# Kernel optimization log

Measured on AMD Instinct MI355X. Metric: run time of the kernel, lower is better.

The kernel has to match this reference:

```python
import jax, jax.numpy as jnp
import numpy as np

HIDDEN = 1024
NEG_INF = jnp.float32(-1e7)


def setup_inputs() -> dict:
    key = jax.random.key(0)
    ks = jax.random.split(key, 9)
    B, S, H = 4, 2048, HIDDEN
    std = 1.0 / np.sqrt(H)
    return {
        "queries": jax.random.normal(ks[0], (B, S, H), jnp.float32),
        "keys": jax.random.normal(ks[1], (B, S, H), jnp.float32),
        "values": jax.random.normal(ks[2], (B, S, H), jnp.float32),
        "Wq": jax.random.uniform(ks[3], (H, H), jnp.float32, -std, std),
        "bq": jax.random.uniform(ks[4], (H,), jnp.float32, -std, std),
        "Wk": jax.random.uniform(ks[5], (H, H), jnp.float32, -std, std),
        "bk": jax.random.uniform(ks[6], (H,), jnp.float32, -std, std),
        "Wv": jax.random.uniform(ks[7], (H, H), jnp.float32, -std, std),
        "bv": jax.random.uniform(ks[8], (H,), jnp.float32, -std, std),
    }


def reference(queries, keys, values, Wq, bq, Wk, bk, Wv, bv):
    # q,k,v: (B, S, H) linear projections (torch Linear: x @ W.T + b)
    q = jnp.einsum('bth,oh->bto', queries, Wq) + bq
    k = jnp.einsum('bsh,oh->bso', keys, Wk) + bk
    v = jnp.einsum('bsh,oh->bso', values, Wv) + bv
    scale = jax.lax.rsqrt(jnp.float32(q.shape[-1] * 0 + Wq.shape[0]))
    # scores[b, s, t] = <k_s, q_t> * scale   (key index s, query index t)
    scores = jnp.einsum('bsh,bth->bst', k, q) * scale
    S, T = scores.shape[1], scores.shape[2]
    # torch.tril(ones * -1e7, diagonal=-1): add -1e7 where s > t (strictly lower)
    mask = jnp.where(jnp.arange(S)[:, None] > jnp.arange(T)[None, :], NEG_INF, 0.0)
    attn = jax.nn.softmax(scores + mask, axis=1)  # softmax over key dim (dim=1)
    context = jnp.einsum('bst,bsh->bth', attn, v)  # (B, T, H)
    return context, attn
```

## Files before the change

kernel.cpp:

```cpp
#include <hip/hip_runtime.h>
#include <math.h>

typedef __bf16 bf16x8 __attribute__((ext_vector_type(8)));
typedef __bf16 bf16x4 __attribute__((ext_vector_type(4)));
typedef float f32x4 __attribute__((ext_vector_type(4)));

#define HD 1024
#define SEQ 2048
#define NB 4
#define WEL (HD * HD)

__device__ inline bf16x8 load8cvt(const __bf16* p) { return *(const bf16x8*)p; }
__device__ inline bf16x8 load8cvt(const float* p) {
    f32x4 a = *(const f32x4*)p;
    f32x4 b = *(const f32x4*)(p + 4);
    bf16x8 r;
#pragma unroll
    for (int i = 0; i < 4; ++i) { r[i] = (__bf16)a[i]; r[i + 4] = (__bf16)b[i]; }
    return r;
}

__device__ inline f32x4 load4f(const float* p) { return *(const f32x4*)p; }
__device__ inline f32x4 load4f(const __bf16* p) {
    bf16x4 v = *(const bf16x4*)p;
    f32x4 r;
#pragma unroll
    for (int i = 0; i < 4; ++i) r[i] = (float)v[i];
    return r;
}

__device__ inline void gld_lds16(const void* g, void* l) {
    __builtin_amdgcn_global_load_lds(
        (const __attribute__((address_space(1))) unsigned int*)g,
        (__attribute__((address_space(3))) unsigned int*)l, 16, 0, 0);
}

template <typename T>
__device__ inline void stage_tile(const T* __restrict__ G, int ld, __bf16* s, int tid)
{
    const int r  = tid >> 3;
    const int co = ((tid & 7) ^ (r & 7)) * 8;
    if constexpr (sizeof(T) == 2) {
        __bf16* dst = s + (tid >> 6) * 512;
#pragma unroll
        for (int c = 0; c < 4; ++c)
            gld_lds16(G + (long)(c * 32 + r) * ld + co, dst + c * 2048);
    } else {
#pragma unroll
        for (int c = 0; c < 4; ++c)
            *(bf16x8*)(s + c * 2048 + tid * 8) = load8cvt(G + (long)(c * 32 + r) * ld + co);
    }
}

__device__ inline bf16x8 frag_read(const __bf16* s, int row, int c)
{
    return *(const bf16x8*)&s[row * 64 + ((c ^ (row & 7)) * 8)];
}

__device__ inline void mfma_ktile(const __bf16* __restrict__ sa,
                                  const __bf16* __restrict__ sb,
                                  int wm, int wn, int l15, int quad,
                                  f32x4 (&acc)[4][4])
{
#pragma unroll
    for (int kk = 0; kk < 64; kk += 32) {
        const int c8 = quad + (kk >> 3);
        bf16x8 af[4], bf[4];
#pragma unroll
        for (int i = 0; i < 4; ++i)
            af[i] = frag_read(sa, wm + i * 16 + l15, c8);
#pragma unroll
        for (int j = 0; j < 4; ++j)
            bf[j] = frag_read(sb, wn + j * 16 + l15, c8);
#pragma unroll
        for (int i = 0; i < 4; ++i)
#pragma unroll
            for (int j = 0; j < 4; ++j)
                acc[i][j] = __builtin_amdgcn_mfma_f32_16x16x32_bf16(af[i], bf[j], acc[i][j], 0, 0, 0);
    }
}

struct Proj3 {
    const void* A[3];
    const void* W[3];
    const float* bias[3];
    __bf16* C[3];
    int vtmask;
};

template <typename TA, typename TW>
__global__ __launch_bounds__(256) void gemm_proj(Proj3 p)
{
    __shared__ __bf16 sA[2][128 * 64];
    __shared__ __bf16 sB[2][128 * 64];

    const int tid = threadIdx.x;
    const int L = blockIdx.x;
    const int per = gridDim.x >> 3;
    const int wrk = (L & 7) * per + (L >> 3);
    const int n0 = (wrk & 7) * 128;
    const int m0 = ((wrk >> 3) & 63) * 128;
    const int z  = wrk >> 9;
    const bool vt = (p.vtmask >> z) & 1;

    const TA* Ag = (const TA*)p.A[z] + (long)m0 * HD;
    const TW* Wg = (const TW*)p.W[z] + (long)n0 * HD;
    const float* bias = p.bias[z];
    __bf16* C = p.C[z];

    const int lane = tid & 63;
    const int l15  = lane & 15;
    const int quad = lane >> 4;
    const int wave = tid >> 6;
    const int wm = (wave >> 1) * 64;
    const int wn = (wave & 1) * 64;

    f32x4 acc[4][4];
    const f32x4 zero = {0.f, 0.f, 0.f, 0.f};
#pragma unroll
    for (int i = 0; i < 4; ++i)
#pragma unroll
        for (int j = 0; j < 4; ++j) acc[i][j] = zero;

    stage_tile(Ag, HD, sA[0], tid);
    stage_tile(Wg, HD, sB[0], tid);
    __syncthreads();

    int cur = 0;
    for (int kc = 0; kc < HD; kc += 64) {
        const int nxt = kc + 64;
        if (nxt < HD) {
            stage_tile(Ag + nxt, HD, sA[cur ^ 1], tid);
            stage_tile(Wg + nxt, HD, sB[cur ^ 1], tid);
        }
        mfma_ktile(sA[cur], sB[cur], wm, wn, l15, quad, acc);
        __syncthreads();
        cur ^= 1;
    }

#pragma unroll
    for (int j = 0; j < 4; ++j) {
        const int col = n0 + wn + j * 16 + l15;
        const float bv = bias[col];
#pragma unroll
        for (int i = 0; i < 4; ++i) {
#pragma unroll
            for (int r = 0; r < 4; ++r) {
                const int row = m0 + wm + i * 16 + quad * 4 + r;
                const float v = acc[i][j][r] + bv;
                if (vt) {
                    C[(((long)(row >> 11) * HD) + col) * SEQ + (row & (SEQ - 1))] = (__bf16)v;
                } else {
                    C[(long)row * HD + col] = (__bf16)v;
                }
            }
        }
    }
}

template <bool TRI, bool CKLIM, bool EXPSUM, typename OutT>
__global__ __launch_bounds__(256) void gemm_bt(
    const __bf16* __restrict__ A, long strideA, int lda,
    const __bf16* __restrict__ B, long strideB, int ldb,
    OutT* __restrict__ C, long strideC, int ldc,
    float* __restrict__ gsum,
    int K, float alpha)
{
    __shared__ __bf16 sA[2][128 * 64];
    __shared__ __bf16 sB[2][128 * 64];
    __shared__ float csum[128];

    const int tid = threadIdx.x;
    const int L = blockIdx.x;
    const int per = gridDim.x >> 3;
    const int wrk = (L & 7) * per + (L >> 3);
    int n0, m0, z;
    if (TRI) {
        const int Lt = wrk % 136;
        z = wrk / 136;
        int tb = (int)((sqrtf(8.f * Lt + 1.f) - 1.f) * 0.5f);
        while ((tb + 1) * (tb + 2) / 2 <= Lt) ++tb;
        while (tb * (tb + 1) / 2 > Lt) --tb;
        const int sb = Lt - tb * (tb + 1) / 2;
        n0 = tb * 128;
        m0 = sb * 128;
    } else {
        n0 = (wrk & 7) * 128;
        m0 = ((wrk >> 3) & 15) * 128;
        z  = wrk >> 7;
    }

    const __bf16* Ag = A + (long)z * strideA + (long)m0 * lda;
    const __bf16* Bg = B + (long)z * strideB + (long)n0 * ldb;
    C += (long)z * strideC;
    if (EXPSUM) {
        gsum += (long)z * SEQ;
        if (tid < 128) csum[tid] = 0.f;
    }

    const int lane = tid & 63;
    const int l15  = lane & 15;
    const int quad = lane >> 4;
    const int wave = tid >> 6;
    const int wm = (wave >> 1) * 64;
    const int wn = (wave & 1) * 64;

    f32x4 acc[4][4];
    const f32x4 zero = {0.f, 0.f, 0.f, 0.f};
#pragma unroll
    for (int i = 0; i < 4; ++i)
#pragma unroll
        for (int j = 0; j < 4; ++j) acc[i][j] = zero;

    const int Kend = CKLIM ? min(K, m0 + 128) : K;

    stage_tile(Ag, lda, sA[0], tid);
    stage_tile(Bg, ldb, sB[0], tid);
    __syncthreads();

    int cur = 0;
    for (int kc = 0; kc < Kend; kc += 64) {
        const int nxt = kc + 64;
        if (nxt < Kend) {
            stage_tile(Ag + nxt, lda, sA[cur ^ 1], tid);
            stage_tile(Bg + nxt, ldb, sB[cur ^ 1], tid);
        }
        mfma_ktile(sA[cur], sB[cur], wm, wn, l15, quad, acc);
        __syncthreads();
        cur ^= 1;
    }

#pragma unroll
    for (int j = 0; j < 4; ++j) {
        const int col = n0 + wn + j * 16 + l15;
        float part = 0.f;
#pragma unroll
        for (int i = 0; i < 4; ++i) {
#pragma unroll
            for (int r = 0; r < 4; ++r) {
                const int row = m0 + wm + i * 16 + quad * 4 + r;
                float v = acc[i][j][r] * alpha;
                if (EXPSUM) {
                    v = __expf(v);
                    if (row <= col) part += v;
                }
                C[(long)row * ldc + col] = (OutT)v;
            }
        }
        if (EXPSUM) atomicAdd(&csum[wn + j * 16 + l15], part);
    }
    if (EXPSUM) {
        __syncthreads();
        if (tid < 128) atomicAdd(&gsum[n0 + tid], csum[tid]);
    }
}

template <typename ET>
__global__ __launch_bounds__(256) void scale_emit(
    const ET* __restrict__ E, float* __restrict__ Out,
    const float* __restrict__ csum, __bf16* __restrict__ AT)
{
    __shared__ __bf16 tile[64][65];
    const int b = blockIdx.z;
    const int t0 = blockIdx.x * 128;
    const int s0 = blockIdx.y * 128;
    const ET* Eb = E + (long)b * SEQ * SEQ;
    float* Ob = Out + (long)b * SEQ * SEQ;
    __bf16* Ab = AT + (long)b * SEQ * SEQ;
    const int tid = threadIdx.x;

    if (s0 > t0 + 127) {
        const f32x4 z4 = {0.f, 0.f, 0.f, 0.f};
        const int c4 = (tid & 31) * 4;
        for (int r = tid >> 5; r < 128; r += 8)
            *(f32x4*)&Ob[(long)(s0 + r) * SEQ + t0 + c4] = z4;
        return;
    }

#pragma unroll
    for (int ds = 0; ds < 2; ++ds) {
#pragma unroll
        for (int dt = 0; dt < 2; ++dt) {
            const int ss = s0 + ds * 64, tt = t0 + dt * 64;
            const int c4 = (tid & 15) * 4;
            const int tcol = tt + c4;
            const f32x4 sv = *(const f32x4*)&csum[(long)b * SEQ + tcol];
            f32x4 inv;
#pragma unroll
            for (int k = 0; k < 4; ++k) inv[k] = 1.0f / sv[k];
#pragma unroll
            for (int r0 = 0; r0 < 64; r0 += 16) {
                const int s = ss + r0 + (tid >> 4);
                f32x4 e = load4f(&Eb[(long)s * SEQ + tcol]);
                f32x4 p;
#pragma unroll
                for (int k = 0; k < 4; ++k)
                    p[k] = (s <= tcol + k) ? e[k] * inv[k] : 0.f;
                *(f32x4*)&Ob[(long)s * SEQ + tcol] = p;
#pragma unroll
                for (int k = 0; k < 4; ++k)
                    tile[r0 + (tid >> 4)][c4 + k] = (__bf16)p[k];
            }
            __syncthreads();
            const int tr = tid >> 2;
            const int sc = (tid & 3) * 16;
            __bf16 v[16];
#pragma unroll
            for (int jj = 0; jj < 16; ++jj) v[jj] = tile[sc + jj][tr];
            *(bf16x8*)&Ab[(long)(tt + tr) * SEQ + ss + sc]     = *(bf16x8*)v;
            *(bf16x8*)&Ab[(long)(tt + tr) * SEQ + ss + sc + 8] = *(bf16x8*)(v + 8);
            __syncthreads();
        }
    }
}

struct CvtJob { const float* in; __bf16* out; int nblk; };
struct Cvt6 { CvtJob j[6]; };
__global__ __launch_bounds__(256) void cvt_bf16(Cvt6 c)
{
    const CvtJob jb = c.j[blockIdx.y];
    if ((int)blockIdx.x >= jb.nblk) return;
    const long i = ((long)blockIdx.x * 256 + threadIdx.x) * 8;
    *(bf16x8*)&jb.out[i] = load8cvt(&jb.in[i]);
}

extern "C" void kernel_launch(void* const* d_in, const int* in_sizes, int n_in,
                              void* d_out, int out_size, void* d_ws, size_t ws_size,
                              hipStream_t stream)
{
    const float* queries = (const float*)d_in[0];
    const float* keys    = (const float*)d_in[1];
    const float* values  = (const float*)d_in[2];
    const float* Wq = (const float*)d_in[3];
    const float* bq = (const float*)d_in[4];
    const float* Wk = (const float*)d_in[5];
    const float* bk = (const float*)d_in[6];
    const float* Wv = (const float*)d_in[7];
    const float* bv = (const float*)d_in[8];

    const long tokens = (long)NB * SEQ;
    const long pe = tokens * HD;
    const size_t SLOT = (size_t)pe * sizeof(__bf16);
    const int ABLK = (int)(pe / 2048);
    const int WBLK = WEL / 2048;

    float* outCtx  = (float*)d_out;
    float* outAttn = outCtx + tokens * HD;
    float* colsum = outCtx;
    __bf16* wb = (__bf16*)outAttn;
    __bf16* Wqb = wb, *Wkb = wb + WEL, *Wvb = wb + 2 * WEL;

    const dim3 blk(256);
    hipMemsetAsync(colsum, 0, (size_t)NB * SEQ * sizeof(float), stream);

    char* w = (char*)d_ws;
    __bf16 *qp, *kp, *vT, *attnT;

    bool ebig = false;
    __bf16* Ebf = nullptr;

    if (ws_size >= 6 * SLOT) {
        __bf16* xq = (__bf16*)w;
        __bf16* xk = (__bf16*)(w + SLOT);
        __bf16* xv = (__bf16*)(w + 2 * SLOT);
        qp = (__bf16*)(w + 3 * SLOT);
        kp = (__bf16*)(w + 4 * SLOT);
        vT = (__bf16*)(w + 5 * SLOT);
        Ebf = (__bf16*)w;
        attnT = (__bf16*)(w + 2 * SLOT);
        ebig = true;

        Cvt6 cv = {{{queries, xq, ABLK}, {keys, xk, ABLK}, {values, xv, ABLK},
                    {Wq, Wqb, WBLK}, {Wk, Wkb, WBLK}, {Wv, Wvb, WBLK}}};
        cvt_bf16<<<dim3(ABLK, 6), blk, 0, stream>>>(cv);
        Proj3 pj = {{xq, xk, xv}, {Wqb, Wkb, Wvb}, {bq, bk, bv}, {qp, kp, vT}, 4};
        gemm_proj<__bf16, __bf16><<<dim3(512 * 3), blk, 0, stream>>>(pj);
    } else if (ws_size >= 4 * SLOT) {
        __bf16* x0 = (__bf16*)w;
        qp = (__bf16*)(w + SLOT);
        kp = (__bf16*)(w + 2 * SLOT);
        __bf16* x1 = (__bf16*)(w + 3 * SLOT);
        vT = x1;
        attnT = (__bf16*)d_ws;

        Cvt6 cv = {{{queries, x0, ABLK}, {keys, x1, ABLK},
                    {Wq, Wqb, WBLK}, {Wk, Wkb, WBLK}, {Wv, Wvb, WBLK},
                    {nullptr, nullptr, 0}}};
        cvt_bf16<<<dim3(ABLK, 5), blk, 0, stream>>>(cv);
        Proj3 pqk = {{x0, x1, nullptr}, {Wqb, Wkb, nullptr}, {bq, bk, nullptr},
                     {qp, kp, nullptr}, 0};
        gemm_proj<__bf16, __bf16><<<dim3(512 * 2), blk, 0, stream>>>(pqk);
        Cvt6 cvv = {{{values, x0, ABLK}, {nullptr, nullptr, 0}, {nullptr, nullptr, 0},
                     {nullptr, nullptr, 0}, {nullptr, nullptr, 0}, {nullptr, nullptr, 0}}};
        cvt_bf16<<<dim3(ABLK, 1), blk, 0, stream>>>(cvv);
        Proj3 pv = {{x0, nullptr, nullptr}, {Wvb, nullptr, nullptr},
                    {bv, nullptr, nullptr}, {vT, nullptr, nullptr}, 1};
        gemm_proj<__bf16, __bf16><<<dim3(512), blk, 0, stream>>>(pv);
    } else {
        qp = (__bf16*)w;
        kp = (__bf16*)(w + SLOT);
        vT = (__bf16*)(w + 2 * SLOT);
        attnT = (__bf16*)d_ws;
        Proj3 pj = {{queries, keys, values}, {Wq, Wk, Wv}, {bq, bk, bv},
                    {qp, kp, vT}, 4};
        gemm_proj<float, float><<<dim3(512 * 3), blk, 0, stream>>>(pj);
    }

    if (ebig) {
        gemm_bt<true, false, true, __bf16><<<dim3(544), blk, 0, stream>>>(
            kp, (long)SEQ * HD, HD, qp, (long)SEQ * HD, HD,
            Ebf, (long)SEQ * SEQ, SEQ, colsum, HD, 0.03125f);
        scale_emit<__bf16><<<dim3(SEQ / 128, SEQ / 128, NB), blk, 0, stream>>>(
            Ebf, outAttn, colsum, attnT);
    } else {
        gemm_bt<true, false, true, float><<<dim3(544), blk, 0, stream>>>(
            kp, (long)SEQ * HD, HD, qp, (long)SEQ * HD, HD,
            outAttn, (long)SEQ * SEQ, SEQ, colsum, HD, 0.03125f);
        scale_emit<float><<<dim3(SEQ / 128, SEQ / 128, NB), blk, 0, stream>>>(
            outAttn, outAttn, colsum, attnT);
    }

    gemm_bt<false, true, false, float><<<dim3(512), blk, 0, stream>>>(
        attnT, (long)SEQ * SEQ, SEQ, vT, (long)HD * SEQ, SEQ,
        outCtx, (long)SEQ * HD, HD, nullptr, SEQ, 1.0f);
}
```

Before: 377.0 us.

## Use 256x256 tiled 8-wave GEMM with swizzled LDS for projections and scores

Adds a 256x256 output-tile GEMM mainloop with 512 threads, 128KB of dynamic LDS, XOR-swizzled half-k staging and a phased schedule built from explicit vmcnt waits, barriers and setprio. This mainloop replaces the 128x128 kernels for the QKV projections and for the causal score GEMM, which now maps blocks onto the 36 upper-triangular 256-tiles per batch. The goal is higher data reuse per block and better MFMA/load overlap. In exchange it uses far fewer blocks (384 and 144), and the hand-tuned wait counts are fragile.

```diff
diff --git a/kernel.cpp b/kernel.cpp
--- a/kernel.cpp
+++ b/kernel.cpp
@@ -77,6 +77,87 @@
 #pragma unroll
             for (int j = 0; j < 4; ++j)
                 acc[i][j] = __builtin_amdgcn_mfma_f32_16x16x32_bf16(af[i], bf[j], acc[i][j], 0, 0, 0);
+    }
+}
+
+__device__ __forceinline__ bf16x8 frag8(const __bf16* s, int row, int quad)
+{
+    return *(const bf16x8*)&s[row * 32 + ((quad ^ ((row >> 1) & 3)) * 8)];
+}
+
+__device__ __forceinline__ void stage_half(const __bf16* __restrict__ G, int ld,
+                                           __bf16* s, int tid)
+{
+    const int row = tid >> 2;
+    const int csw = ((tid & 3) ^ ((tid >> 3) & 3)) * 8;
+    __bf16* dst = s + (tid >> 6) * 512;
+    gld_lds16(G + (long)row * ld + csw, dst);
+    gld_lds16(G + (long)(row + 128) * ld + csw, dst + 4096);
+}
+
+#define VM4 asm volatile("s_waitcnt vmcnt(4)" ::: "memory")
+#define VM0 asm volatile("s_waitcnt vmcnt(0)" ::: "memory")
+
+#define PHASE(SAH, SBH, IH, LOADB, STAGE_STMT, VM_STMT)                         \
+    {                                                                           \
+        bf16x8 af_[4];                                                          \
+        _Pragma("unroll") for (int i_ = 0; i_ < 4; ++i_)                        \
+            af_[i_] = frag8(SAH, wr * 128 + ((IH) * 4 + i_) * 16 + l15, quad);  \
+        if (LOADB) {                                                            \
+            _Pragma("unroll") for (int j_ = 0; j_ < 4; ++j_)                    \
+                bf[j_] = frag8(SBH, wc * 64 + j_ * 16 + l15, quad);             \
+        }                                                                       \
+        STAGE_STMT;                                                             \
+        VM_STMT;                                                                \
+        __builtin_amdgcn_s_barrier();                                           \
+        asm volatile("s_waitcnt lgkmcnt(0)" ::: "memory");                      \
+        __builtin_amdgcn_sched_barrier(0);                                      \
+        __builtin_amdgcn_s_setprio(1);                                          \
+        _Pragma("unroll") for (int i_ = 0; i_ < 4; ++i_)                        \
+        _Pragma("unroll") for (int j_ = 0; j_ < 4; ++j_)                        \
+            acc[(IH) * 4 + i_][j_] = __builtin_amdgcn_mfma_f32_16x16x32_bf16(   \
+                af_[i_], bf[j_], acc[(IH) * 4 + i_][j_], 0, 0, 0);              \
+        __builtin_amdgcn_s_setprio(0);                                          \
+        __builtin_amdgcn_s_barrier();                                           \
+    }
+
+__device__ __forceinline__ void kloop256(
+    const __bf16* __restrict__ Ag, int lda,
+    const __bf16* __restrict__ Bg, int ldb,
+    int NT, __bf16* lds, int tid, f32x4 (&acc)[8][4])
+{
+    const int lane = tid & 63;
+    const int l15  = lane & 15;
+    const int quad = lane >> 4;
+    const int wave = tid >> 6;
+    const int wr = wave >> 2;
+    const int wc = wave & 3;
+
+    auto SA = [&](int b, int h) { return lds + (b * 2 + h) * 8192; };
+    auto SB = [&](int b, int h) { return lds + 32768 + (b * 2 + h) * 8192; };
+    auto stA = [&](int t, int h) {
+        if (t < NT) stage_half(Ag + t * 64 + h * 32, lda, SA(t & 1, h), tid);
+    };
+    auto stB = [&](int t, int h) {
+        if (t < NT) stage_half(Bg + t * 64 + h * 32, ldb, SB(t & 1, h), tid);
+    };
+
+    stA(0, 0); stB(0, 0); stA(0, 1); stB(0, 1); stA(1, 0); stB(1, 0);
+    VM4;
+    __builtin_amdgcn_s_barrier();
+
+    bf16x8 bf[4];
+    for (int c = 0; c < NT; c += 2) {
+        const bool last = (c + 2 >= NT);
+        PHASE(SA(0, 0), SB(0, 0), 0, true,  (stA(c + 1, 1)), (void)0);
+        PHASE(SA(0, 0), SB(0, 0), 1, false, (stB(c + 1, 1)), (void)0);
+        PHASE(SA(0, 1), SB(0, 1), 0, true,  (stA(c + 2, 0)), (void)0);
+        PHASE(SA(0, 1), SB(0, 1), 1, false, (stB(c + 2, 0)),
+              if (last) { VM0; } else { VM4; });
+        PHASE(SA(1, 0), SB(1, 0), 0, true,  (stA(c + 2, 1)), (void)0);
+        PHASE(SA(1, 0), SB(1, 0), 1, false, (stB(c + 2, 1)), (void)0);
+        PHASE(SA(1, 1), SB(1, 1), 0, true,  (stA(c + 3, 0)), (void)0);
+        PHASE(SA(1, 1), SB(1, 1), 1, false, (stB(c + 3, 0)), VM4);
     }
 }
 
@@ -88,66 +169,45 @@
     int vtmask;
 };
 
-template <typename TA, typename TW>
-__global__ __launch_bounds__(256) void gemm_proj(Proj3 p)
-{
-    __shared__ __bf16 sA[2][128 * 64];
-    __shared__ __bf16 sB[2][128 * 64];
-
+__global__ __launch_bounds__(512, 2) void gemm_proj256(Proj3 p)
+{
+    extern __shared__ __bf16 lds[];
     const int tid = threadIdx.x;
     const int L = blockIdx.x;
     const int per = gridDim.x >> 3;
     const int wrk = (L & 7) * per + (L >> 3);
-    const int n0 = (wrk & 7) * 128;
-    const int m0 = ((wrk >> 3) & 63) * 128;
-    const int z  = wrk >> 9;
+    const int r  = wrk & 127;
+    const int z  = wrk >> 7;
+    const int n0 = (r & 3) * 256;
+    const int m0 = (r >> 2) * 256;
     const bool vt = (p.vtmask >> z) & 1;
 
-    const TA* Ag = (const TA*)p.A[z] + (long)m0 * HD;
-    const TW* Wg = (const TW*)p.W[z] + (long)n0 * HD;
+    const __bf16* Ag = (const __bf16*)p.A[z] + (long)m0 * HD;
+    const __bf16* Wg = (const __bf16*)p.W[z] + (long)n0 * HD;
     const float* bias = p.bias[z];
     __bf16* C = p.C[z];
 
-    const int lane = tid & 63;
-    const int l15  = lane & 15;
-    const int quad = lane >> 4;
-    const int wave = tid >> 6;
-    const int wm = (wave >> 1) * 64;
-    const int wn = (wave & 1) * 64;
-
-    f32x4 acc[4][4];
+    f32x4 acc[8][4];
     const f32x4 zero = {0.f, 0.f, 0.f, 0.f};
 #pragma unroll
-    for (int i = 0; i < 4; ++i)
+    for (int i = 0; i < 8; ++i)
 #pragma unroll
         for (int j = 0; j < 4; ++j) acc[i][j] = zero;
 
-    stage_tile(Ag, HD, sA[0], tid);
-    stage_tile(Wg, HD, sB[0], tid);
-    __syncthreads();
-
-    int cur = 0;
-    for (int kc = 0; kc < HD; kc += 64) {
-        const int nxt = kc + 64;
-        if (nxt < HD) {
-            stage_tile(Ag + nxt, HD, sA[cur ^ 1], tid);
-            stage_tile(Wg + nxt, HD, sB[cur ^ 1], tid);
-        }
-        mfma_ktile(sA[cur], sB[cur], wm, wn, l15, quad, acc);
-        __syncthreads();
-        cur ^= 1;
-    }
-
+    kloop256(Ag, HD, Wg, HD, HD / 64, lds, tid, acc);
+
+    const int lane = tid & 63, l15 = lane & 15, quad = lane >> 4;
+    const int wave = tid >> 6, wr = wave >> 2, wc = wave & 3;
 #pragma unroll
     for (int j = 0; j < 4; ++j) {
-        const int col = n0 + wn + j * 16 + l15;
+        const int col = n0 + wc * 64 + j * 16 + l15;
         const float bv = bias[col];
 #pragma unroll
-        for (int i = 0; i < 4; ++i) {
-#pragma unroll
-            for (int r = 0; r < 4; ++r) {
-                const int row = m0 + wm + i * 16 + quad * 4 + r;
-                const float v = acc[i][j][r] + bv;
+        for (int i = 0; i < 8; ++i) {
+#pragma unroll
+            for (int rr = 0; rr < 4; ++rr) {
+                const int row = m0 + wr * 128 + i * 16 + quad * 4 + rr;
+                const float v = acc[i][j][rr] + bv;
                 if (vt) {
                     C[(((long)(row >> 11) * HD) + col) * SEQ + (row & (SEQ - 1))] = (__bf16)v;
                 } else {
@@ -156,6 +216,65 @@
             }
         }
     }
+}
+
+template <typename OutT>
+__global__ __launch_bounds__(512, 2) void gemm_sc256(
+    const __bf16* __restrict__ A, const __bf16* __restrict__ B,
+    OutT* __restrict__ C, float* __restrict__ gsum, float alpha)
+{
+    extern __shared__ __bf16 lds[];
+    __shared__ float csum[256];
+    const int tid = threadIdx.x;
+    const int L = blockIdx.x;
+    const int per = gridDim.x >> 3;
+    const int wrk = (L & 7) * per + (L >> 3);
+    const int Lt = wrk % 36;
+    const int z  = wrk / 36;
+    int tb = (int)((sqrtf(8.f * Lt + 1.f) - 1.f) * 0.5f);
+    while ((tb + 1) * (tb + 2) / 2 <= Lt) ++tb;
+    while (tb * (tb + 1) / 2 > Lt) --tb;
+    const int sb = Lt - tb * (tb + 1) / 2;
+    const int n0 = tb * 256;
+    const int m0 = sb * 256;
+
+    const __bf16* Ag = A + (long)z * SEQ * HD + (long)m0 * HD;
+    const __bf16* Bg = B + (long)z * SEQ * HD + (long)n0 * HD;
+    OutT* Cz = C + (long)z * SEQ * SEQ;
+    gsum += (long)z * SEQ;
+
+    if (tid < 256) csum[tid] = 0.f;
+    __syncthreads();
+
+    f32x4 acc[8][4];
+    const f32x4 zero = {0.f, 0.f, 0.f, 0.f};
+#pragma unroll
+    for (int i = 0; i < 8; ++i)
+#pragma unroll
+        for (int j = 0; j < 4; ++j) acc[i][j] = zero;
+
+    kloop256(Ag, HD, Bg, HD, HD / 64, lds, tid, acc);
+
+    const int lane = tid & 63, l15 = lane & 15, quad = lane >> 4;
+    const int wave = tid >> 6, wr = wave >> 2, wc = wave & 3;
+#pragma unroll
+    for (int j = 0; j < 4; ++j) {
+        const int col = n0 + wc * 64 + j * 16 + l15;
+        float part = 0.f;
+#pragma unroll
+        for (int i = 0; i < 8; ++i) {
+#pragma unroll
+            for (int rr = 0; rr < 4; ++rr) {
+                const int row = m0 + wr * 128 + i * 16 + quad * 4 + rr;
+                float v = __expf(acc[i][j][rr] * alpha);
+                if (row <= col) part += v;
+                Cz[(long)row * SEQ + col] = (OutT)v;
+            }
+        }
+        atomicAdd(&csum[wc * 64 + j * 16 + l15], part);
+    }
+    __syncthreads();
+    if (tid < 256) atomicAdd(&gsum[n0 + tid], csum[tid]);
 }
 
 template <bool TRI, bool CKLIM, bool EXPSUM, typename OutT>
@@ -255,6 +374,76 @@
     }
 }
 
+template <typename TA, typename TW>
+__global__ __launch_bounds__(256) void gemm_proj(Proj3 p)
+{
+    __shared__ __bf16 sA[2][128 * 64];
+    __shared__ __bf16 sB[2][128 * 64];
+
+    const int tid = threadIdx.x;
+    const int L = blockIdx.x;
+    const int per = gridDim.x >> 3;
+    const int wrk = (L & 7) * per + (L >> 3);
+    const int n0 = (wrk & 7) * 128;
+    const int m0 = ((wrk >> 3) & 63) * 128;
+    const int z  = wrk >> 9;
+    const bool vt = (p.vtmask >> z) & 1;
+
+    const TA* Ag = (const TA*)p.A[z] + (long)m0 * HD;
+    const TW* Wg = (const TW*)p.W[z] + (long)n0 * HD;
+    const float* bias = p.bias[z];
+    __bf16* C = p.C[z];
+
+    const int lane = tid & 63;
+    const int l15  = lane & 15;
+    const int quad = lane >> 4;
+    const int wave = tid >> 6;
+    const int wm = (wave >> 1) * 64;
+    const int wn = (wave & 1) * 64;
+
+    f32x4 acc[4][4];
+    const f32x4 zero = {0.f, 0.f, 0.f, 0.f};
+#pragma unroll
+    for (int i = 0; i < 4; ++i)
+#pragma unroll
+        for (int j = 0; j < 4; ++j) acc[i][j] = zero;
+
+    stage_tile(Ag, HD, sA[0], tid);
+    stage_tile(Wg, HD, sB[0], tid);
+    __syncthreads();
+
+    int cur = 0;
+    for (int kc = 0; kc < HD; kc += 64) {
+        const int nxt = kc + 64;
+        if (nxt < HD) {
+            stage_tile(Ag + nxt, HD, sA[cur ^ 1], tid);
+            stage_tile(Wg + nxt, HD, sB[cur ^ 1], tid);
+        }
+        mfma_ktile(sA[cur], sB[cur], wm, wn, l15, quad, acc);
+        __syncthreads();
+        cur ^= 1;
+    }
+
+#pragma unroll
+    for (int j = 0; j < 4; ++j) {
+        const int col = n0 + wn + j * 16 + l15;
+        const float bv = bias[col];
+#pragma unroll
+        for (int i = 0; i < 4; ++i) {
+#pragma unroll
+            for (int r = 0; r < 4; ++r) {
+                const int row = m0 + wm + i * 16 + quad * 4 + r;
+                const float v = acc[i][j][r] + bv;
+                if (vt) {
+                    C[(((long)(row >> 11) * HD) + col) * SEQ + (row & (SEQ - 1))] = (__bf16)v;
+                } else {
+                    C[(long)row * HD + col] = (__bf16)v;
+                }
+            }
+        }
+    }
+}
+
 template <typename ET>
 __global__ __launch_bounds__(256) void scale_emit(
     const ET* __restrict__ E, float* __restrict__ Out,
@@ -343,6 +532,18 @@
     const size_t SLOT = (size_t)pe * sizeof(__bf16);
     const int ABLK = (int)(pe / 2048);
     const int WBLK = WEL / 2048;
+    const int LDS256 = 131072;
+
+    static int attr_done = 0;
+    if (!attr_done) {
+        hipFuncSetAttribute((const void*)gemm_proj256,
+                            hipFuncAttributeMaxDynamicSharedMemorySize, LDS256);
+        hipFuncSetAttribute((const void*)gemm_sc256<__bf16>,
+                            hipFuncAttributeMaxDynamicSharedMemorySize, LDS256);
+        hipFuncSetAttribute((const void*)gemm_sc256<float>,
+                            hipFuncAttributeMaxDynamicSharedMemorySize, LDS256);
+        attr_done = 1;
+    }
 
     float* outCtx  = (float*)d_out;
     float* outAttn = outCtx + tokens * HD;
@@ -351,6 +552,7 @@
     __bf16* Wqb = wb, *Wkb = wb + WEL, *Wvb = wb + 2 * WEL;
 
     const dim3 blk(256);
+    const dim3 blk512(512);
     hipMemsetAsync(colsum, 0, (size_t)NB * SEQ * sizeof(float), stream);
 
     char* w = (char*)d_ws;
@@ -374,7 +576,7 @@
                     {Wq, Wqb, WBLK}, {Wk, Wkb, WBLK}, {Wv, Wvb, WBLK}}};
         cvt_bf16<<<dim3(ABLK, 6), blk, 0, stream>>>(cv);
         Proj3 pj = {{xq, xk, xv}, {Wqb, Wkb, Wvb}, {bq, bk, bv}, {qp, kp, vT}, 4};
-        gemm_proj<__bf16, __bf16><<<dim3(512 * 3), blk, 0, stream>>>(pj);
+        gemm_proj256<<<dim3(128 * 3), blk512, LDS256, stream>>>(pj);
     } else if (ws_size >= 4 * SLOT) {
         __bf16* x0 = (__bf16*)w;
         qp = (__bf16*)(w + SLOT);
@@ -389,13 +591,13 @@
         cvt_bf16<<<dim3(ABLK, 5), blk, 0, stream>>>(cv);
         Proj3 pqk = {{x0, x1, nullptr}, {Wqb, Wkb, nullptr}, {bq, bk, nullptr},
                      {qp, kp, nullptr}, 0};
-        gemm_proj<__bf16, __bf16><<<dim3(512 * 2), blk, 0, stream>>>(pqk);
+        gemm_proj256<<<dim3(128 * 2), blk512, LDS256, stream>>>(pqk);
         Cvt6 cvv = {{{values, x0, ABLK}, {nullptr, nullptr, 0}, {nullptr, nullptr, 0},
                      {nullptr, nullptr, 0}, {nullptr, nullptr, 0}, {nullptr, nullptr, 0}}};
         cvt_bf16<<<dim3(ABLK, 1), blk, 0, stream>>>(cvv);
         Proj3 pv = {{x0, nullptr, nullptr}, {Wvb, nullptr, nullptr},
                     {bv, nullptr, nullptr}, {vT, nullptr, nullptr}, 1};
-        gemm_proj<__bf16, __bf16><<<dim3(512), blk, 0, stream>>>(pv);
+        gemm_proj256<<<dim3(128), blk512, LDS256, stream>>>(pv);
     } else {
         qp = (__bf16*)w;
         kp = (__bf16*)(w + SLOT);
@@ -407,15 +609,13 @@
     }
 
     if (ebig) {
-        gemm_bt<true, false, true, __bf16><<<dim3(544), blk, 0, stream>>>(
-            kp, (long)SEQ * HD, HD, qp, (long)SEQ * HD, HD,
-            Ebf, (long)SEQ * SEQ, SEQ, colsum, HD, 0.03125f);
+        gemm_sc256<__bf16><<<dim3(144), blk512, LDS256, stream>>>(
+            kp, qp, Ebf, colsum, 0.03125f);
         scale_emit<__bf16><<<dim3(SEQ / 128, SEQ / 128, NB), blk, 0, stream>>>(
             Ebf, outAttn, colsum, attnT);
     } else {
-        gemm_bt<true, false, true, float><<<dim3(544), blk, 0, stream>>>(
-            kp, (long)SEQ * HD, HD, qp, (long)SEQ * HD, HD,
-            outAttn, (long)SEQ * SEQ, SEQ, colsum, HD, 0.03125f);
+        gemm_sc256<float><<<dim3(144), blk512, LDS256, stream>>>(
+            kp, qp, outAttn, colsum, 0.03125f);
         scale_emit<float><<<dim3(SEQ / 128, SEQ / 128, NB), blk, 0, stream>>>(
             outAttn, outAttn, colsum, attnT);
     }
```

Result: slower. 386.1 us (+2.4%).

## Add 4-stage pipelined projection GEMM and transposed-score attention path

Applied to the files above, without the earlier changes.

The projection GEMM is replaced by a version with a 4-deep async LDS pipeline over 32-wide K tiles, explicit vmcnt waits and raised MFMA priority, to hide global-load latency. For the large-workspace path, scores are now computed transposed (q rows, k columns), so the row sums come from in-register shuffles and the context GEMM reads the unnormalized exp matrix directly, applying 1/sum in its epilogue. This drops the separate bf16 transposed-attention copy, and the attention emit becomes a normalize-and-transpose pass. It adds more kernels and code paths, and normalizing after accumulation slightly changes rounding.

```diff
diff --git a/kernel.cpp b/kernel.cpp
--- a/kernel.cpp
+++ b/kernel.cpp
@@ -35,6 +35,8 @@
         (__attribute__((address_space(3))) unsigned int*)l, 16, 0, 0);
 }
 
+#define VMC(N) asm volatile("s_waitcnt vmcnt(" #N ")" ::: "memory")
+
 template <typename T>
 __device__ inline void stage_tile(const T* __restrict__ G, int ld, __bf16* s, int tid)
 {
@@ -78,6 +80,20 @@
             for (int j = 0; j < 4; ++j)
                 acc[i][j] = __builtin_amdgcn_mfma_f32_16x16x32_bf16(af[i], bf[j], acc[i][j], 0, 0, 0);
     }
+}
+
+__device__ inline void stage32(const __bf16* __restrict__ G, int ld, __bf16* s, int tid)
+{
+    const int r = tid >> 2;
+    const int c = ((tid & 3) ^ ((r >> 1) & 3)) * 8;
+    __bf16* dst = s + (tid >> 6) * 512;
+    gld_lds16(G + (long)r * ld + c, dst);
+    gld_lds16(G + (long)(r + 64) * ld + c, dst + 2048);
+}
+
+__device__ __forceinline__ bf16x8 frag32(const __bf16* s, int row, int quad)
+{
+    return *(const bf16x8*)&s[row * 32 + ((quad ^ ((row >> 1) & 3)) * 8)];
 }
 
 struct Proj3 {
@@ -88,11 +104,10 @@
     int vtmask;
 };
 
-template <typename TA, typename TW>
-__global__ __launch_bounds__(256) void gemm_proj(Proj3 p)
-{
-    __shared__ __bf16 sA[2][128 * 64];
-    __shared__ __bf16 sB[2][128 * 64];
+__global__ __launch_bounds__(256) void gemm_proj_dp(Proj3 p)
+{
+    __shared__ __bf16 sA[4][128 * 32];
+    __shared__ __bf16 sB[4][128 * 32];
 
     const int tid = threadIdx.x;
     const int L = blockIdx.x;
@@ -103,14 +118,12 @@
     const int z  = wrk >> 9;
     const bool vt = (p.vtmask >> z) & 1;
 
-    const TA* Ag = (const TA*)p.A[z] + (long)m0 * HD;
-    const TW* Wg = (const TW*)p.W[z] + (long)n0 * HD;
+    const __bf16* Ag = (const __bf16*)p.A[z] + (long)m0 * HD;
+    const __bf16* Wg = (const __bf16*)p.W[z] + (long)n0 * HD;
     const float* bias = p.bias[z];
     __bf16* C = p.C[z];
 
-    const int lane = tid & 63;
-    const int l15  = lane & 15;
-    const int quad = lane >> 4;
+    const int lane = tid & 63, l15 = lane & 15, quad = lane >> 4;
     const int wave = tid >> 6;
     const int wm = (wave >> 1) * 64;
     const int wn = (wave & 1) * 64;
@@ -122,20 +135,36 @@
 #pragma unroll
         for (int j = 0; j < 4; ++j) acc[i][j] = zero;
 
-    stage_tile(Ag, HD, sA[0], tid);
-    stage_tile(Wg, HD, sB[0], tid);
-    __syncthreads();
-
-    int cur = 0;
-    for (int kc = 0; kc < HD; kc += 64) {
-        const int nxt = kc + 64;
-        if (nxt < HD) {
-            stage_tile(Ag + nxt, HD, sA[cur ^ 1], tid);
-            stage_tile(Wg + nxt, HD, sB[cur ^ 1], tid);
-        }
-        mfma_ktile(sA[cur], sB[cur], wm, wn, l15, quad, acc);
-        __syncthreads();
-        cur ^= 1;
+    stage32(Ag,      HD, sA[0], tid); stage32(Wg,      HD, sB[0], tid);
+    stage32(Ag + 32, HD, sA[1], tid); stage32(Wg + 32, HD, sB[1], tid);
+    stage32(Ag + 64, HD, sA[2], tid); stage32(Wg + 64, HD, sB[2], tid);
+
+    const int NT = HD / 32;
+    for (int t = 0; t < NT; ++t) {
+        if (t + 3 < NT) {
+            stage32(Ag + (t + 3) * 32, HD, sA[(t + 3) & 3], tid);
+            stage32(Wg + (t + 3) * 32, HD, sB[(t + 3) & 3], tid);
+            VMC(12);
+        } else if (t + 2 < NT) { VMC(8); }
+        else if (t + 1 < NT)   { VMC(4); }
+        else                   { VMC(0); }
+        __builtin_amdgcn_s_barrier();
+        __builtin_amdgcn_sched_barrier(0);
+        const __bf16* sa = sA[t & 3];
+        const __bf16* sb = sB[t & 3];
+        bf16x8 af[4], bg[4];
+#pragma unroll
+        for (int i = 0; i < 4; ++i) af[i] = frag32(sa, wm + i * 16 + l15, quad);
+#pragma unroll
+        for (int j = 0; j < 4; ++j) bg[j] = frag32(sb, wn + j * 16 + l15, quad);
+        __builtin_amdgcn_s_setprio(1);
+#pragma unroll
+        for (int i = 0; i < 4; ++i)
+#pragma unroll
+            for (int j = 0; j < 4; ++j)
+                acc[i][j] = __builtin_amdgcn_mfma_f32_16x16x32_bf16(af[i], bg[j], acc[i][j], 0, 0, 0);
+        __builtin_amdgcn_s_setprio(0);
+        __builtin_amdgcn_s_barrier();
     }
 
 #pragma unroll
@@ -154,6 +183,218 @@
                     C[(long)row * HD + col] = (__bf16)v;
                 }
             }
+        }
+    }
+}
+
+template <typename OutT>
+__global__ __launch_bounds__(256) void gemm_sc(
+    const __bf16* __restrict__ A, const __bf16* __restrict__ B,
+    OutT* __restrict__ C, float* __restrict__ gsum, float alpha)
+{
+    __shared__ __bf16 s1[2][128 * 64];
+    __shared__ __bf16 s2[2][128 * 64];
+    __shared__ float csum[128];
+
+    const int tid = threadIdx.x;
+    const int L = blockIdx.x;
+    const int per = gridDim.x >> 3;
+    const int wrk = (L & 7) * per + (L >> 3);
+    const int Lt = wrk % 136;
+    const int z  = wrk / 136;
+    int tb = (int)((sqrtf(8.f * Lt + 1.f) - 1.f) * 0.5f);
+    while ((tb + 1) * (tb + 2) / 2 <= Lt) ++tb;
+    while (tb * (tb + 1) / 2 > Lt) --tb;
+    const int sb = Lt - tb * (tb + 1) / 2;
+    const int m0 = tb * 128;
+    const int n0 = sb * 128;
+
+    const __bf16* Ag = A + (long)z * SEQ * HD + (long)m0 * HD;
+    const __bf16* Bg = B + (long)z * SEQ * HD + (long)n0 * HD;
+    C += (long)z * SEQ * SEQ;
+    gsum += (long)z * SEQ;
+    if (tid < 128) csum[tid] = 0.f;
+
+    const int lane = tid & 63, l15 = lane & 15, quad = lane >> 4;
+    const int wave = tid >> 6;
+    const int wm = (wave >> 1) * 64;
+    const int wn = (wave & 1) * 64;
+
+    f32x4 acc[4][4];
+    const f32x4 zero = {0.f, 0.f, 0.f, 0.f};
+#pragma unroll
+    for (int i = 0; i < 4; ++i)
+#pragma unroll
+        for (int j = 0; j < 4; ++j) acc[i][j] = zero;
+
+    stage_tile(Ag, HD, s1[0], tid);
+    stage_tile(Bg, HD, s2[0], tid);
+    __syncthreads();
+    int cur = 0;
+    for (int kc = 0; kc < HD; kc += 64) {
+        const int nxt = kc + 64;
+        if (nxt < HD) {
+            stage_tile(Ag + nxt, HD, s1[cur ^ 1], tid);
+            stage_tile(Bg + nxt, HD, s2[cur ^ 1], tid);
+        }
+        mfma_ktile(s1[cur], s2[cur], wm, wn, l15, quad, acc);
+        __syncthreads();
+        cur ^= 1;
+    }
+
+    float rsum[4][4];
+#pragma unroll
+    for (int i = 0; i < 4; ++i)
+#pragma unroll
+        for (int r = 0; r < 4; ++r) rsum[i][r] = 0.f;
+
+#pragma unroll
+    for (int j = 0; j < 4; ++j) {
+        const int col = n0 + wn + j * 16 + l15;
+#pragma unroll
+        for (int i = 0; i < 4; ++i) {
+#pragma unroll
+            for (int r = 0; r < 4; ++r) {
+                const int row = m0 + wm + i * 16 + quad * 4 + r;
+                const float e = (col <= row) ? __expf(acc[i][j][r] * alpha) : 0.f;
+                C[(long)row * SEQ + col] = (OutT)e;
+                rsum[i][r] += e;
+            }
+        }
+    }
+#pragma unroll
+    for (int i = 0; i < 4; ++i) {
+#pragma unroll
+        for (int r = 0; r < 4; ++r) {
+            float v = rsum[i][r];
+            v += __shfl_xor(v, 1); v += __shfl_xor(v, 2);
+            v += __shfl_xor(v, 4); v += __shfl_xor(v, 8);
+            if (l15 == 0) atomicAdd(&csum[wm + i * 16 + quad * 4 + r], v);
+        }
+    }
+    __syncthreads();
+    if (tid < 128) atomicAdd(&gsum[m0 + tid], csum[tid]);
+}
+
+__global__ __launch_bounds__(256) void gemm_ctx(
+    const __bf16* __restrict__ A, const __bf16* __restrict__ B,
+    float* __restrict__ C, const float* __restrict__ gsum)
+{
+    __shared__ __bf16 s1[2][128 * 64];
+    __shared__ __bf16 s2[2][128 * 64];
+    __shared__ float rs[128];
+
+    const int tid = threadIdx.x;
+    const int L = blockIdx.x;
+    const int per = gridDim.x >> 3;
+    const int wrk = (L & 7) * per + (L >> 3);
+    const int n0 = (wrk & 7) * 128;
+    const int m0 = ((wrk >> 3) & 15) * 128;
+    const int z  = wrk >> 7;
+
+    const __bf16* Ag = A + (long)z * SEQ * SEQ + (long)m0 * SEQ;
+    const __bf16* Bg = B + (long)z * HD * SEQ + (long)n0 * SEQ;
+    C += (long)z * SEQ * HD;
+    if (tid < 128) rs[tid] = gsum[(long)z * SEQ + m0 + tid];
+
+    const int lane = tid & 63, l15 = lane & 15, quad = lane >> 4;
+    const int wave = tid >> 6;
+    const int wm = (wave >> 1) * 64;
+    const int wn = (wave & 1) * 64;
+
+    f32x4 acc[4][4];
+    const f32x4 zero = {0.f, 0.f, 0.f, 0.f};
+#pragma unroll
+    for (int i = 0; i < 4; ++i)
+#pragma unroll
+        for (int j = 0; j < 4; ++j) acc[i][j] = zero;
+
+    const int Kend = m0 + 128;
+
+    stage_tile(Ag, SEQ, s1[0], tid);
+    stage_tile(Bg, SEQ, s2[0], tid);
+    __syncthreads();
+    int cur = 0;
+    for (int kc = 0; kc < Kend; kc += 64) {
+        const int nxt = kc + 64;
+        if (nxt < Kend) {
+            stage_tile(Ag + nxt, SEQ, s1[cur ^ 1], tid);
+            stage_tile(Bg + nxt, SEQ, s2[cur ^ 1], tid);
+        }
+        mfma_ktile(s1[cur], s2[cur], wm, wn, l15, quad, acc);
+        __syncthreads();
+        cur ^= 1;
+    }
+
+    float invr[4][4];
+#pragma unroll
+    for (int i = 0; i < 4; ++i)
+#pragma unroll
+        for (int r = 0; r < 4; ++r)
+            invr[i][r] = 1.0f / rs[wm + i * 16 + quad * 4 + r];
+
+#pragma unroll
+    for (int j = 0; j < 4; ++j) {
+        const int col = n0 + wn + j * 16 + l15;
+#pragma unroll
+        for (int i = 0; i < 4; ++i) {
+#pragma unroll
+            for (int r = 0; r < 4; ++r) {
+                const int row = m0 + wm + i * 16 + quad * 4 + r;
+                C[(long)row * HD + col] = acc[i][j][r] * invr[i][r];
+            }
+        }
+    }
+}
+
+__global__ __launch_bounds__(256) void emit_attn(
+    const __bf16* __restrict__ Et, float* __restrict__ Out,
+    const float* __restrict__ csum)
+{
+    __shared__ float tile[64][65];
+    const int b = blockIdx.z;
+    const int t0 = blockIdx.x * 128;
+    const int s0 = blockIdx.y * 128;
+    const __bf16* Eb = Et + (long)b * SEQ * SEQ;
+    float* Ob = Out + (long)b * SEQ * SEQ;
+    const int tid = threadIdx.x;
+
+    if (s0 > t0 + 127) {
+        const f32x4 z4 = {0.f, 0.f, 0.f, 0.f};
+        const int c4 = (tid & 31) * 4;
+        for (int r = tid >> 5; r < 128; r += 8)
+            *(f32x4*)&Ob[(long)(s0 + r) * SEQ + t0 + c4] = z4;
+        return;
+    }
+
+#pragma unroll
+    for (int dt = 0; dt < 2; ++dt) {
+#pragma unroll
+        for (int dsb = 0; dsb < 2; ++dsb) {
+            const int tt = t0 + dt * 64, ss = s0 + dsb * 64;
+            const int c4 = (tid & 15) * 4;
+#pragma unroll
+            for (int r0 = 0; r0 < 64; r0 += 16) {
+                const int tl = r0 + (tid >> 4);
+                const float inv = 1.0f / csum[(long)b * SEQ + tt + tl];
+                f32x4 e = load4f(&Eb[(long)(tt + tl) * SEQ + ss + c4]);
+#pragma unroll
+                for (int k = 0; k < 4; ++k) tile[tl][c4 + k] = e[k] * inv;
+            }
+            __syncthreads();
+            const int sl = tid >> 2;
+            const int tc = (tid & 3) * 16;
+            float v[16];
+#pragma unroll
+            for (int jj = 0; jj < 16; ++jj) v[jj] = tile[tc + jj][sl];
+#pragma unroll
+            for (int q = 0; q < 4; ++q) {
+                f32x4 ov;
+#pragma unroll
+                for (int k = 0; k < 4; ++k) ov[k] = v[q * 4 + k];
+                *(f32x4*)&Ob[(long)(ss + sl) * SEQ + tt + tc + q * 4] = ov;
+            }
+            __syncthreads();
         }
     }
 }
@@ -255,6 +496,76 @@
     }
 }
 
+template <typename TA, typename TW>
+__global__ __launch_bounds__(256) void gemm_proj(Proj3 p)
+{
+    __shared__ __bf16 sA[2][128 * 64];
+    __shared__ __bf16 sB[2][128 * 64];
+
+    const int tid = threadIdx.x;
+    const int L = blockIdx.x;
+    const int per = gridDim.x >> 3;
+    const int wrk = (L & 7) * per + (L >> 3);
+    const int n0 = (wrk & 7) * 128;
+    const int m0 = ((wrk >> 3) & 63) * 128;
+    const int z  = wrk >> 9;
+    const bool vt = (p.vtmask >> z) & 1;
+
+    const TA* Ag = (const TA*)p.A[z] + (long)m0 * HD;
+    const TW* Wg = (const TW*)p.W[z] + (long)n0 * HD;
+    const float* bias = p.bias[z];
+    __bf16* C = p.C[z];
+
+    const int lane = tid & 63;
+    const int l15  = lane & 15;
+    const int quad = lane >> 4;
+    const int wave = tid >> 6;
+    const int wm = (wave >> 1) * 64;
+    const int wn = (wave & 1) * 64;
+
+    f32x4 acc[4][4];
+    const f32x4 zero = {0.f, 0.f, 0.f, 0.f};
+#pragma unroll
+    for (int i = 0; i < 4; ++i)
+#pragma unroll
+        for (int j = 0; j < 4; ++j) acc[i][j] = zero;
+
+    stage_tile(Ag, HD, sA[0], tid);
+    stage_tile(Wg, HD, sB[0], tid);
+    __syncthreads();
+
+    int cur = 0;
+    for (int kc = 0; kc < HD; kc += 64) {
+        const int nxt = kc + 64;
+        if (nxt < HD) {
+            stage_tile(Ag + nxt, HD, sA[cur ^ 1], tid);
+            stage_tile(Wg + nxt, HD, sB[cur ^ 1], tid);
+        }
+        mfma_ktile(sA[cur], sB[cur], wm, wn, l15, quad, acc);
+        __syncthreads();
+        cur ^= 1;
+    }
+
+#pragma unroll
+    for (int j = 0; j < 4; ++j) {
+        const int col = n0 + wn + j * 16 + l15;
+        const float bv = bias[col];
+#pragma unroll
+        for (int i = 0; i < 4; ++i) {
+#pragma unroll
+            for (int r = 0; r < 4; ++r) {
+                const int row = m0 + wm + i * 16 + quad * 4 + r;
+                const float v = acc[i][j][r] + bv;
+                if (vt) {
+                    C[(((long)(row >> 11) * HD) + col) * SEQ + (row & (SEQ - 1))] = (__bf16)v;
+                } else {
+                    C[(long)row * HD + col] = (__bf16)v;
+                }
+            }
+        }
+    }
+}
+
 template <typename ET>
 __global__ __launch_bounds__(256) void scale_emit(
     const ET* __restrict__ E, float* __restrict__ Out,
@@ -346,18 +657,12 @@
 
     float* outCtx  = (float*)d_out;
     float* outAttn = outCtx + tokens * HD;
-    float* colsum = outCtx;
     __bf16* wb = (__bf16*)outAttn;
     __bf16* Wqb = wb, *Wkb = wb + WEL, *Wvb = wb + 2 * WEL;
 
     const dim3 blk(256);
-    hipMemsetAsync(colsum, 0, (size_t)NB * SEQ * sizeof(float), stream);
-
     char* w = (char*)d_ws;
-    __bf16 *qp, *kp, *vT, *attnT;
-
-    bool ebig = false;
-    __bf16* Ebf = nullptr;
+    __bf16 *qp, *kp, *vT;
 
     if (ws_size >= 6 * SLOT) {
         __bf16* xq = (__bf16*)w;
@@ -366,22 +671,29 @@
         qp = (__bf16*)(w + 3 * SLOT);
         kp = (__bf16*)(w + 4 * SLOT);
         vT = (__bf16*)(w + 5 * SLOT);
-        Ebf = (__bf16*)w;
-        attnT = (__bf16*)(w + 2 * SLOT);
-        ebig = true;
+        __bf16* Ebf = (__bf16*)w;
+        float* colsum = (float*)(w + 2 * SLOT);
 
         Cvt6 cv = {{{queries, xq, ABLK}, {keys, xk, ABLK}, {values, xv, ABLK},
                     {Wq, Wqb, WBLK}, {Wk, Wkb, WBLK}, {Wv, Wvb, WBLK}}};
         cvt_bf16<<<dim3(ABLK, 6), blk, 0, stream>>>(cv);
         Proj3 pj = {{xq, xk, xv}, {Wqb, Wkb, Wvb}, {bq, bk, bv}, {qp, kp, vT}, 4};
-        gemm_proj<__bf16, __bf16><<<dim3(512 * 3), blk, 0, stream>>>(pj);
+        gemm_proj_dp<<<dim3(512 * 3), blk, 0, stream>>>(pj);
+
+        hipMemsetAsync(colsum, 0, (size_t)NB * SEQ * sizeof(float), stream);
+        gemm_sc<__bf16><<<dim3(544), blk, 0, stream>>>(qp, kp, Ebf, colsum, 0.03125f);
+        emit_attn<<<dim3(SEQ / 128, SEQ / 128, NB), blk, 0, stream>>>(
+            Ebf, outAttn, colsum);
+        gemm_ctx<<<dim3(512), blk, 0, stream>>>(Ebf, vT, outCtx, colsum);
     } else if (ws_size >= 4 * SLOT) {
+        float* colsum = outCtx;
+        hipMemsetAsync(colsum, 0, (size_t)NB * SEQ * sizeof(float), stream);
         __bf16* x0 = (__bf16*)w;
         qp = (__bf16*)(w + SLOT);
         kp = (__bf16*)(w + 2 * SLOT);
         __bf16* x1 = (__bf16*)(w + 3 * SLOT);
         vT = x1;
-        attnT = (__bf16*)d_ws;
+        __bf16* attnT = (__bf16*)d_ws;
 
         Cvt6 cv = {{{queries, x0, ABLK}, {keys, x1, ABLK},
                     {Wq, Wqb, WBLK}, {Wk, Wkb, WBLK}, {Wv, Wvb, WBLK},
@@ -389,38 +701,40 @@
         cvt_bf16<<<dim3(ABLK, 5), blk, 0, stream>>>(cv);
         Proj3 pqk = {{x0, x1, nullptr}, {Wqb, Wkb, nullptr}, {bq, bk, nullptr},
                      {qp, kp, nullptr}, 0};
-        gemm_proj<__bf16, __bf16><<<dim3(512 * 2), blk, 0, stream>>>(pqk);
+        gemm_proj_dp<<<dim3(512 * 2), blk, 0, stream>>>(pqk);
         Cvt6 cvv = {{{values, x0, ABLK}, {nullptr, nullptr, 0}, {nullptr, nullptr, 0},
                      {nullptr, nullptr, 0}, {nullptr, nullptr, 0}, {nullptr, nullptr, 0}}};
         cvt_bf16<<<dim3(ABLK, 1), blk, 0, stream>>>(cvv);
         Proj3 pv = {{x0, nullptr, nullptr}, {Wvb, nullptr, nullptr},
                     {bv, nullptr, nullptr}, {vT, nullptr, nullptr}, 1};
-        gemm_proj<__bf16, __bf16><<<dim3(512), blk, 0, stream>>>(pv);
-    } else {
-        qp = (__bf16*)w;
-        kp = (__bf16*)(w + SLOT);
-        vT = (__bf16*)(w + 2 * SLOT);
-        attnT = (__bf16*)d_ws;
-        Proj3 pj = {{queries, keys, values}, {Wq, Wk, Wv}, {bq, bk, bv},
-                    {qp, kp, vT}, 4};
-        gemm_proj<float, float><<<dim3(512 * 3), blk, 0, stream>>>(pj);
-    }
-
-    if (ebig) {
-        gemm_bt<true, false, true, __bf16><<<dim3(544), blk, 0, stream>>>(
-            kp, (long)SEQ * HD, HD, qp, (long)SEQ * HD, HD,
-            Ebf, (long)SEQ * SEQ, SEQ, colsum, HD, 0.03125f);
-        scale_emit<__bf16><<<dim3(SEQ / 128, SEQ / 128, NB), blk, 0, stream>>>(
-            Ebf, outAttn, colsum, attnT);
-    } else {
+        gemm_proj_dp<<<dim3(512), blk, 0, stream>>>(pv);
+
         gemm_bt<true, false, true, float><<<dim3(544), blk, 0, stream>>>(
             kp, (long)SEQ * HD, HD, qp, (long)SEQ * HD, HD,
             outAttn, (long)SEQ * SEQ, SEQ, colsum, HD, 0.03125f);
         scale_emit<float><<<dim3(SEQ / 128, SEQ / 128, NB), blk, 0, stream>>>(
             outAttn, outAttn, colsum, attnT);
-    }
-
-    gemm_bt<false, true, false, float><<<dim3(512), blk, 0, stream>>>(
-        attnT, (long)SEQ * SEQ, SEQ, vT, (long)HD * SEQ, SEQ,
-        outCtx, (long)SEQ * HD, HD, nullptr, SEQ, 1.0f);
-}
+        gemm_bt<false, true, false, float><<<dim3(512), blk, 0, stream>>>(
+            attnT, (long)SEQ * SEQ, SEQ, vT, (long)HD * SEQ, SEQ,
+            outCtx, (long)SEQ * HD, HD, nullptr, SEQ, 1.0f);
+    } else {
+        float* colsum = outCtx;
+        hipMemsetAsync(colsum, 0, (size_t)NB * SEQ * sizeof(float), stream);
+        qp = (__bf16*)w;
+        kp = (__bf16*)(w + SLOT);
+        vT = (__bf16*)(w + 2 * SLOT);
+        __bf16* attnT = (__bf16*)d_ws;
+        Proj3 pj = {{queries, keys, values}, {Wq, Wk, Wv}, {bq, bk, bv},
+                    {qp, kp, vT}, 4};
+        gemm_proj<float, float><<<dim3(512 * 3), blk, 0, stream>>>(pj);
+
+        gemm_bt<true, false, true, float><<<dim3(544), blk, 0, stream>>>(
+            kp, (long)SEQ * HD, HD, qp, (long)SEQ * HD, HD,
+            outAttn, (long)SEQ * SEQ, SEQ, colsum, HD, 0.03125f);
+        scale_emit<float><<<dim3(SEQ / 128, SEQ / 128, NB), blk, 0, stream>>>(
+            outAttn, outAttn, colsum, attnT);
+        gemm_bt<false, true, false, float><<<dim3(512), blk, 0, stream>>>(
+            attnT, (long)SEQ * SEQ, SEQ, vT, (long)HD * SEQ, SEQ,
+            outCtx, (long)SEQ * HD, HD, nullptr, SEQ, 1.0f);
+    }
+}
```

After: 399.5 us. 6.0% more time.
